# Optimization experiments

Hardware: AMD Instinct MI355X
Metric: run time of the kernel (lower is better)

## Reference

```python
import jax, jax.numpy as jnp
import numpy as np

UNITS = 50

def setup_inputs() -> dict:
    key = jax.random.key(0)
    ks = jax.random.split(key, 6)
    B, T, F = 4096, 128, 64
    scale = 0.1
    return {
        "x": jax.random.normal(ks[0], (B, T, F), dtype=jnp.float32),
        "W": jax.random.normal(ks[1], (F, 3 * UNITS), dtype=jnp.float32) * scale,
        "U": jax.random.normal(ks[2], (UNITS, 3 * UNITS), dtype=jnp.float32) * scale,
        "b": jax.random.normal(ks[3], (2, 3 * UNITS), dtype=jnp.float32) * scale,
        "Wd": jax.random.normal(ks[4], (UNITS, 1), dtype=jnp.float32) * scale,
        "bd": jnp.zeros((1,), dtype=jnp.float32),
    }

def reference(x, W, U, b, Wd, bd):
    # Keras GRU, reset_after=True, activation=relu, recurrent_activation=sigmoid.
    B, T, F = x.shape
    u = UNITS
    # Precompute input projections for all timesteps: [B,T,3u]
    xp = jnp.einsum('btf,fk->btk', x, W) + b[0]
    xp = jnp.moveaxis(xp, 1, 0)  # [T,B,3u]
    bi = b[1]

    def step(h, xt):
        hp = h @ U + bi                     # [B,3u]
        xz, xr, xh = xt[:, :u], xt[:, u:2*u], xt[:, 2*u:]
        hz, hr, hh = hp[:, :u], hp[:, u:2*u], hp[:, 2*u:]
        z = jax.nn.sigmoid(xz + hz)
        r = jax.nn.sigmoid(xr + hr)
        hcand = jax.nn.relu(xh + r * hh)
        h_new = z * h + (1.0 - z) * hcand
        return h_new, None

    h0 = jnp.zeros((B, u), dtype=x.dtype)
    hT, _ = jax.lax.scan(step, h0, xp)
    # Dropout is identity at inference; Dense head:
    return hT @ Wd + bd
```

## Files before the change

kernel.cpp:

```cpp
#include <hip/hip_runtime.h>
#include <math.h>

typedef _Float16 v8h __attribute__((ext_vector_type(8)));
typedef float v4f __attribute__((ext_vector_type(4)));

#define UNITS    50
#define K3       150
#define FDIM     64
#define TSTEPS   128
#define BATCH    4096
#define NB       16
#define H16S     72
#define H32S     52

#if __has_builtin(__builtin_amdgcn_exp2f)
__device__ __forceinline__ float fast_exp2(float x) { return __builtin_amdgcn_exp2f(x); }
#else
__device__ __forceinline__ float fast_exp2(float x) { return exp2f(x); }
#endif
#if __has_builtin(__builtin_amdgcn_rcpf)
__device__ __forceinline__ float fast_rcp(float x) { return __builtin_amdgcn_rcpf(x); }
#else
__device__ __forceinline__ float fast_rcp(float x) { return 1.0f / x; }
#endif

__global__ __launch_bounds__(256, 1)
void gru_4w(const float* __restrict__ x, const float* __restrict__ W,
            const float* __restrict__ U, const float* __restrict__ bv,
            const float* __restrict__ Wd, const float* __restrict__ bd,
            float* __restrict__ out) {
    __shared__ _Float16 hs16[2][NB * H16S];
    __shared__ float    hs32[NB * H32S];

    const int tid  = threadIdx.x;
    const int nt   = tid >> 6;
    const int lane = tid & 63;
    const int n    = lane & 15;
    const int quad = lane >> 4;
    const int b0   = blockIdx.x * NB;
    const int c    = nt * 16 + n;

    for (int i = tid; i < NB * H16S; i += 256) {
        _Float16 v = ((i % H16S) == 50) ? (_Float16)1.f : (_Float16)0.f;
        hs16[0][i] = v;
        hs16[1][i] = v;
    }

    v8h Bz[4], Br[4], Bh[4];
    #pragma unroll
    for (int kt = 0; kt < 4; ++kt) {
        v8h fz, fr, fh;
        #pragma unroll
        for (int j = 0; j < 8; ++j) {
            const int k = kt * 32 + quad * 8 + j;
            float vz = 0.f, vr = 0.f, vh = 0.f;
            if (c < UNITS) {
                if (k < FDIM) {
                    vz = W[k * K3 + c];
                    vr = W[k * K3 + 50 + c];
                    vh = W[k * K3 + 100 + c];
                } else if (k < FDIM + UNITS) {
                    const int ur = k - FDIM;
                    vz = U[ur * K3 + c];
                    vr = U[ur * K3 + 50 + c];
                    vh = U[ur * K3 + 100 + c];
                } else if (k == FDIM + UNITS) {
                    vh = bv[250 + c];
                }
            }
            fz[j] = (_Float16)vz; fr[j] = (_Float16)vr; fh[j] = (_Float16)vh;
        }
        Bz[kt] = fz; Br[kt] = fr; Bh[kt] = fh;
    }

    const float CE = -1.44269504f;
    float bzc = 0.f, brc = 0.f, bx = 0.f;
    if (c < UNITS) {
        bzc = CE * (bv[c]      + bv[150 + c]);
        brc = CE * (bv[50 + c] + bv[200 + c]);
        bx  = bv[100 + c];
    }

    v4f h32 = {0.f, 0.f, 0.f, 0.f};

    const float* xbase = x + ((size_t)(b0 + n) * TSTEPS) * FDIM + quad * 8;
    v4f px0 = *(const v4f*)(xbase + 0);
    v4f px1 = *(const v4f*)(xbase + 4);
    v4f px2 = *(const v4f*)(xbase + 32);
    v4f px3 = *(const v4f*)(xbase + 36);

    __syncthreads();

    for (int t = 0; t < TSTEPS; ++t) {
        const _Float16* hrd = hs16[t & 1];
        _Float16*       hwr = hs16[(t + 1) & 1];

        v8h A0, A1;
        #pragma unroll
        for (int j = 0; j < 4; ++j) {
            A0[j]     = (_Float16)px0[j];
            A0[j + 4] = (_Float16)px1[j];
            A1[j]     = (_Float16)px2[j];
            A1[j + 4] = (_Float16)px3[j];
        }
        v8h A2 = *(const v8h*)(&hrd[n * H16S + quad * 8]);
        v8h A3 = *(const v8h*)(&hrd[n * H16S + 32 + quad * 8]);

        if (t + 1 < TSTEPS) {
            const float* xp = xbase + (size_t)(t + 1) * FDIM;
            px0 = *(const v4f*)(xp + 0);
            px1 = *(const v4f*)(xp + 4);
            px2 = *(const v4f*)(xp + 32);
            px3 = *(const v4f*)(xp + 36);
        }

        const v4f zero4 = {0.f, 0.f, 0.f, 0.f};
        v4f ax = {bx, bx, bx, bx};
        v4f az = __builtin_amdgcn_mfma_f32_16x16x32_f16(A0, Bz[0], zero4, 0, 0, 0);
        az     = __builtin_amdgcn_mfma_f32_16x16x32_f16(A1, Bz[1], az,    0, 0, 0);
        v4f ar = __builtin_amdgcn_mfma_f32_16x16x32_f16(A0, Br[0], zero4, 0, 0, 0);
        ar     = __builtin_amdgcn_mfma_f32_16x16x32_f16(A1, Br[1], ar,    0, 0, 0);
        ax     = __builtin_amdgcn_mfma_f32_16x16x32_f16(A0, Bh[0], ax,    0, 0, 0);
        ax     = __builtin_amdgcn_mfma_f32_16x16x32_f16(A1, Bh[1], ax,    0, 0, 0);
        az     = __builtin_amdgcn_mfma_f32_16x16x32_f16(A2, Bz[2], az,    0, 0, 0);
        az     = __builtin_amdgcn_mfma_f32_16x16x32_f16(A3, Bz[3], az,    0, 0, 0);
        ar     = __builtin_amdgcn_mfma_f32_16x16x32_f16(A2, Br[2], ar,    0, 0, 0);
        ar     = __builtin_amdgcn_mfma_f32_16x16x32_f16(A3, Br[3], ar,    0, 0, 0);
        v4f ah = __builtin_amdgcn_mfma_f32_16x16x32_f16(A2, Bh[2], zero4, 0, 0, 0);
        ah     = __builtin_amdgcn_mfma_f32_16x16x32_f16(A3, Bh[3], ah,    0, 0, 0);

        #pragma unroll
        for (int r = 0; r < 4; ++r) {
            const float ez = fast_exp2(fmaf(az[r], CE, bzc));
            const float er = fast_exp2(fmaf(ar[r], CE, brc));
            const float pz = 1.f + ez;
            const float pr = 1.f + er;
            const float d  = fast_rcp(pz * pr);
            const float zg = d * pr;
            const float rg = d * pz;
            const float hc = fmaxf(fmaf(rg, ah[r], ax[r]), 0.f);
            const float hn = fmaf(zg, h32[r] - hc, hc);
            h32[r] = hn;
            if (c < UNITS)
                hwr[(quad * 4 + r) * H16S + c] = (_Float16)hn;
        }
        __syncthreads();
    }

    if (c < UNITS) {
        #pragma unroll
        for (int r = 0; r < 4; ++r)
            hs32[(quad * 4 + r) * H32S + c] = h32[r];
    }
    __syncthreads();
    if (tid < NB) {
        float acc = bd[0];
        #pragma unroll
        for (int u = 0; u < UNITS; ++u)
            acc = fmaf(hs32[tid * H32S + u], Wd[u], acc);
        out[b0 + tid] = acc;
    }
}

extern "C" void kernel_launch(void* const* d_in, const int* in_sizes, int n_in,
                              void* d_out, int out_size, void* d_ws, size_t ws_size,
                              hipStream_t stream) {
    const float* x    = (const float*)d_in[0];
    const float* W    = (const float*)d_in[1];
    const float* U    = (const float*)d_in[2];
    const float* bv   = (const float*)d_in[3];
    const float* Wd   = (const float*)d_in[4];
    const float* bd   = (const float*)d_in[5];
    float* out = (float*)d_out;

    dim3 grid(BATCH / NB);
    dim3 block(256);
    gru_4w<<<grid, block, 0, stream>>>(x, W, U, bv, Wd, bd, out);
}
```

Baseline: 272.6 us.

## Software-pipeline input projection MFMAs one step ahead and deepen x prefetch

Moves the x-dependent MFMAs for step t+1 into step t, after the recurrent MFMAs are issued, so they overlap the gate math and stay off the h-dependent critical path. The x prefetch now reaches two steps ahead using alternating register buffers and a loop unrolled by two. __syncthreads is replaced by an explicit lgkmcnt wait plus s_barrier and sched_barrier. This costs extra registers for the prefetched x and the partial accumulators, and the hand-written barrier is a correctness risk if any memory ordering was relied on.

```diff
diff --git a/kernel.cpp b/kernel.cpp
--- a/kernel.cpp
+++ b/kernel.cpp
@@ -84,50 +84,72 @@
     v4f h32 = {0.f, 0.f, 0.f, 0.f};
 
     const float* xbase = x + ((size_t)(b0 + n) * TSTEPS) * FDIM + quad * 8;
-    v4f px0 = *(const v4f*)(xbase + 0);
-    v4f px1 = *(const v4f*)(xbase + 4);
-    v4f px2 = *(const v4f*)(xbase + 32);
-    v4f px3 = *(const v4f*)(xbase + 36);
+
+    v4f az_x, ar_x, ax_x;
+    auto xpart = [&](const v4f& q0, const v4f& q1, const v4f& q2, const v4f& q3) {
+        v8h A0, A1;
+        #pragma unroll
+        for (int j = 0; j < 4; ++j) {
+            A0[j]     = (_Float16)q0[j];
+            A0[j + 4] = (_Float16)q1[j];
+            A1[j]     = (_Float16)q2[j];
+            A1[j + 4] = (_Float16)q3[j];
+        }
+        const v4f zero4 = {0.f, 0.f, 0.f, 0.f};
+        az_x = __builtin_amdgcn_mfma_f32_16x16x32_f16(A0, Bz[0], zero4, 0, 0, 0);
+        az_x = __builtin_amdgcn_mfma_f32_16x16x32_f16(A1, Bz[1], az_x,  0, 0, 0);
+        ar_x = __builtin_amdgcn_mfma_f32_16x16x32_f16(A0, Br[0], zero4, 0, 0, 0);
+        ar_x = __builtin_amdgcn_mfma_f32_16x16x32_f16(A1, Br[1], ar_x,  0, 0, 0);
+        v4f axi = {bx, bx, bx, bx};
+        ax_x = __builtin_amdgcn_mfma_f32_16x16x32_f16(A0, Bh[0], axi,  0, 0, 0);
+        ax_x = __builtin_amdgcn_mfma_f32_16x16x32_f16(A1, Bh[1], ax_x, 0, 0, 0);
+    };
+
+    {
+        v4f q0 = *(const v4f*)(xbase + 0);
+        v4f q1 = *(const v4f*)(xbase + 4);
+        v4f q2 = *(const v4f*)(xbase + 32);
+        v4f q3 = *(const v4f*)(xbase + 36);
+        xpart(q0, q1, q2, q3);
+    }
+    v4f pxO[4], pxE[4];
+    {
+        const float* x1 = xbase + (size_t)1 * FDIM;
+        pxO[0] = *(const v4f*)(x1 + 0);  pxO[1] = *(const v4f*)(x1 + 4);
+        pxO[2] = *(const v4f*)(x1 + 32); pxO[3] = *(const v4f*)(x1 + 36);
+        const float* x2 = xbase + (size_t)2 * FDIM;
+        pxE[0] = *(const v4f*)(x2 + 0);  pxE[1] = *(const v4f*)(x2 + 4);
+        pxE[2] = *(const v4f*)(x2 + 32); pxE[3] = *(const v4f*)(x2 + 36);
+    }
 
     __syncthreads();
 
-    for (int t = 0; t < TSTEPS; ++t) {
+    auto step = [&](int t, v4f (&px)[4]) {
         const _Float16* hrd = hs16[t & 1];
         _Float16*       hwr = hs16[(t + 1) & 1];
 
-        v8h A0, A1;
-        #pragma unroll
-        for (int j = 0; j < 4; ++j) {
-            A0[j]     = (_Float16)px0[j];
-            A0[j + 4] = (_Float16)px1[j];
-            A1[j]     = (_Float16)px2[j];
-            A1[j + 4] = (_Float16)px3[j];
-        }
         v8h A2 = *(const v8h*)(&hrd[n * H16S + quad * 8]);
         v8h A3 = *(const v8h*)(&hrd[n * H16S + 32 + quad * 8]);
 
-        if (t + 1 < TSTEPS) {
-            const float* xp = xbase + (size_t)(t + 1) * FDIM;
-            px0 = *(const v4f*)(xp + 0);
-            px1 = *(const v4f*)(xp + 4);
-            px2 = *(const v4f*)(xp + 32);
-            px3 = *(const v4f*)(xp + 36);
-        }
-
         const v4f zero4 = {0.f, 0.f, 0.f, 0.f};
-        v4f ax = {bx, bx, bx, bx};
-        v4f az = __builtin_amdgcn_mfma_f32_16x16x32_f16(A0, Bz[0], zero4, 0, 0, 0);
-        az     = __builtin_amdgcn_mfma_f32_16x16x32_f16(A1, Bz[1], az,    0, 0, 0);
-        v4f ar = __builtin_amdgcn_mfma_f32_16x16x32_f16(A0, Br[0], zero4, 0, 0, 0);
-        ar     = __builtin_amdgcn_mfma_f32_16x16x32_f16(A1, Br[1], ar,    0, 0, 0);
-        ax     = __builtin_amdgcn_mfma_f32_16x16x32_f16(A0, Bh[0], ax,    0, 0, 0);
-        ax     = __builtin_amdgcn_mfma_f32_16x16x32_f16(A1, Bh[1], ax,    0, 0, 0);
-        az     = __builtin_amdgcn_mfma_f32_16x16x32_f16(A2, Bz[2], az,    0, 0, 0);
-        az     = __builtin_amdgcn_mfma_f32_16x16x32_f16(A3, Bz[3], az,    0, 0, 0);
-        ar     = __builtin_amdgcn_mfma_f32_16x16x32_f16(A2, Br[2], ar,    0, 0, 0);
-        ar     = __builtin_amdgcn_mfma_f32_16x16x32_f16(A3, Br[3], ar,    0, 0, 0);
+        v4f az = __builtin_amdgcn_mfma_f32_16x16x32_f16(A2, Bz[2], az_x, 0, 0, 0);
+        az     = __builtin_amdgcn_mfma_f32_16x16x32_f16(A3, Bz[3], az,   0, 0, 0);
+        v4f ar = __builtin_amdgcn_mfma_f32_16x16x32_f16(A2, Br[2], ar_x, 0, 0, 0);
+        ar     = __builtin_amdgcn_mfma_f32_16x16x32_f16(A3, Br[3], ar,   0, 0, 0);
         v4f ah = __builtin_amdgcn_mfma_f32_16x16x32_f16(A2, Bh[2], zero4, 0, 0, 0);
         ah     = __builtin_amdgcn_mfma_f32_16x16x32_f16(A3, Bh[3], ah,    0, 0, 0);
+        v4f ax = ax_x;
+
+        if (t + 1 < TSTEPS) {
+            xpart(px[0], px[1], px[2], px[3]);
+            if (t + 3 < TSTEPS) {
+                const float* xp = xbase + (size_t)(t + 3) * FDIM;
+                px[0] = *(const v4f*)(xp + 0);
+                px[1] = *(const v4f*)(xp + 4);
+                px[2] = *(const v4f*)(xp + 32);
+                px[3] = *(const v4f*)(xp + 36);
+            }
+        }
 
         #pragma unroll
         for (int r = 0; r < 4; ++r) {
@@ -144,7 +166,15 @@
             if (c < UNITS)
                 hwr[(quad * 4 + r) * H16S + c] = (_Float16)hn;
         }
-        __syncthreads();
+
+        asm volatile("s_waitcnt lgkmcnt(0)" ::: "memory");
+        __builtin_amdgcn_s_barrier();
+        __builtin_amdgcn_sched_barrier(0);
+    };
+
+    for (int t = 0; t < TSTEPS; t += 2) {
+        step(t,     pxO);
+        step(t + 1, pxE);
     }
 
     if (c < UNITS) {
```

New measurement: 274.2 us. No clear change (+0.6%).

## Run each batch tile in one wave with transposed MFMA and register-resident state

Applied to the files above, without the earlier changes.

Replaces the 4-wave block, which exchanged the hidden state through shared memory and a barrier every step, with a single 64-lane wave per 16-row batch tile. The GEMM is transposed so the weights act as the A operand and the batch as B, letting each lane's hidden-state outputs feed straight into the next step's B operand without LDS or __syncthreads. The z/r biases are folded into the matmul through a constant-one input, x loads are prefetched two steps ahead with a step pair unrolled, and the dense head is reduced with cross-lane shuffles. The cost is four times as many MFMAs per wave, large register pressure from holding 48 weight fragments, and only one wave per block.

```diff
diff --git a/kernel.cpp b/kernel.cpp
--- a/kernel.cpp
+++ b/kernel.cpp
@@ -10,8 +10,6 @@
 #define TSTEPS   128
 #define BATCH    4096
 #define NB       16
-#define H16S     72
-#define H32S     52
 
 #if __has_builtin(__builtin_amdgcn_exp2f)
 __device__ __forceinline__ float fast_exp2(float x) { return __builtin_amdgcn_exp2f(x); }
@@ -24,142 +22,164 @@
 __device__ __forceinline__ float fast_rcp(float x) { return 1.0f / x; }
 #endif
 
-__global__ __launch_bounds__(256, 1)
-void gru_4w(const float* __restrict__ x, const float* __restrict__ W,
+__global__ __launch_bounds__(64, 1)
+void gru_1w(const float* __restrict__ x, const float* __restrict__ W,
             const float* __restrict__ U, const float* __restrict__ bv,
             const float* __restrict__ Wd, const float* __restrict__ bd,
             float* __restrict__ out) {
-    __shared__ _Float16 hs16[2][NB * H16S];
-    __shared__ float    hs32[NB * H32S];
+    const int lane = threadIdx.x & 63;
+    const int n    = lane & 15;
+    const int q    = lane >> 4;
+    const int b0   = blockIdx.x * NB;
 
-    const int tid  = threadIdx.x;
-    const int nt   = tid >> 6;
-    const int lane = tid & 63;
-    const int n    = lane & 15;
-    const int quad = lane >> 4;
-    const int b0   = blockIdx.x * NB;
-    const int c    = nt * 16 + n;
-
-    for (int i = tid; i < NB * H16S; i += 256) {
-        _Float16 v = ((i % H16S) == 50) ? (_Float16)1.f : (_Float16)0.f;
-        hs16[0][i] = v;
-        hs16[1][i] = v;
+    v8h Az[4][4], Ar[4][4], Ah[4][4];
+    #pragma unroll
+    for (int mt = 0; mt < 4; ++mt) {
+        const int m = mt * 16 + n;
+        const bool mreal = (m < UNITS);
+        #pragma unroll
+        for (int kt = 0; kt < 4; ++kt) {
+            v8h fz, fr, fh;
+            #pragma unroll
+            for (int j = 0; j < 8; ++j) {
+                float vz = 0.f, vr = 0.f, vh = 0.f;
+                if (mreal) {
+                    if (kt < 2) {
+                        const int feat = kt * 32 + q * 8 + j;
+                        vz = W[feat * K3 + m];
+                        vr = W[feat * K3 + 50 + m];
+                        vh = W[feat * K3 + 100 + m];
+                    } else if (kt == 3 && q == 0 && j == 6) {
+                        vz = bv[m]      + bv[150 + m];
+                        vr = bv[50 + m] + bv[200 + m];
+                        vh = bv[250 + m];
+                    } else {
+                        const int u = ((kt - 2) * 2 + (j >> 2)) * 16 + q * 4 + (j & 3);
+                        if (u < UNITS) {
+                            vz = U[u * K3 + m];
+                            vr = U[u * K3 + 50 + m];
+                            vh = U[u * K3 + 100 + m];
+                        }
+                    }
+                }
+                fz[j] = (_Float16)vz; fr[j] = (_Float16)vr; fh[j] = (_Float16)vh;
+            }
+            Az[mt][kt] = fz; Ar[mt][kt] = fr; Ah[mt][kt] = fh;
+        }
     }
 
-    v8h Bz[4], Br[4], Bh[4];
+    v4f bx4[4];
     #pragma unroll
-    for (int kt = 0; kt < 4; ++kt) {
-        v8h fz, fr, fh;
+    for (int mt = 0; mt < 4; ++mt)
         #pragma unroll
-        for (int j = 0; j < 8; ++j) {
-            const int k = kt * 32 + quad * 8 + j;
-            float vz = 0.f, vr = 0.f, vh = 0.f;
-            if (c < UNITS) {
-                if (k < FDIM) {
-                    vz = W[k * K3 + c];
-                    vr = W[k * K3 + 50 + c];
-                    vh = W[k * K3 + 100 + c];
-                } else if (k < FDIM + UNITS) {
-                    const int ur = k - FDIM;
-                    vz = U[ur * K3 + c];
-                    vr = U[ur * K3 + 50 + c];
-                    vh = U[ur * K3 + 100 + c];
-                } else if (k == FDIM + UNITS) {
-                    vh = bv[250 + c];
-                }
-            }
-            fz[j] = (_Float16)vz; fr[j] = (_Float16)vr; fh[j] = (_Float16)vh;
+        for (int r = 0; r < 4; ++r) {
+            const int u = mt * 16 + q * 4 + r;
+            bx4[mt][r] = (u < UNITS) ? bv[100 + u] : 0.f;
         }
-        Bz[kt] = fz; Br[kt] = fr; Bh[kt] = fh;
+
+    const float CE = -1.44269504f;
+
+    v4f h32[4];
+    #pragma unroll
+    for (int mt = 0; mt < 4; ++mt) h32[mt] = v4f{0.f, 0.f, 0.f, 0.f};
+
+    const float* xb = x + ((size_t)(b0 + n) * TSTEPS) * FDIM + q * 8;
+    v4f pxA[4], pxB[4];
+    pxA[0] = *(const v4f*)(xb + 0);  pxA[1] = *(const v4f*)(xb + 4);
+    pxA[2] = *(const v4f*)(xb + 32); pxA[3] = *(const v4f*)(xb + 36);
+    {
+        const float* x1 = xb + (size_t)FDIM;
+        pxB[0] = *(const v4f*)(x1 + 0);  pxB[1] = *(const v4f*)(x1 + 4);
+        pxB[2] = *(const v4f*)(x1 + 32); pxB[3] = *(const v4f*)(x1 + 36);
     }
 
-    const float CE = -1.44269504f;
-    float bzc = 0.f, brc = 0.f, bx = 0.f;
-    if (c < UNITS) {
-        bzc = CE * (bv[c]      + bv[150 + c]);
-        brc = CE * (bv[50 + c] + bv[200 + c]);
-        bx  = bv[100 + c];
+    auto step = [&](int t, v4f (&px)[4]) {
+        v8h B0, B1;
+        #pragma unroll
+        for (int j = 0; j < 4; ++j) {
+            B0[j]     = (_Float16)px[0][j];
+            B0[j + 4] = (_Float16)px[1][j];
+            B1[j]     = (_Float16)px[2][j];
+            B1[j + 4] = (_Float16)px[3][j];
+        }
+        const v4f z4 = {0.f, 0.f, 0.f, 0.f};
+        v4f Cz[4], Cr[4], Chx[4], Chh[4];
+        #pragma unroll
+        for (int mt = 0; mt < 4; ++mt) {
+            Cz[mt]  = __builtin_amdgcn_mfma_f32_16x16x32_f16(Az[mt][0], B0, z4,       0, 0, 0);
+            Cr[mt]  = __builtin_amdgcn_mfma_f32_16x16x32_f16(Ar[mt][0], B0, z4,       0, 0, 0);
+            Chx[mt] = __builtin_amdgcn_mfma_f32_16x16x32_f16(Ah[mt][0], B0, bx4[mt],  0, 0, 0);
+        }
+        #pragma unroll
+        for (int mt = 0; mt < 4; ++mt) {
+            Cz[mt]  = __builtin_amdgcn_mfma_f32_16x16x32_f16(Az[mt][1], B1, Cz[mt],  0, 0, 0);
+            Cr[mt]  = __builtin_amdgcn_mfma_f32_16x16x32_f16(Ar[mt][1], B1, Cr[mt],  0, 0, 0);
+            Chx[mt] = __builtin_amdgcn_mfma_f32_16x16x32_f16(Ah[mt][1], B1, Chx[mt], 0, 0, 0);
+        }
+        if (t + 2 < TSTEPS) {
+            const float* xp = xb + (size_t)(t + 2) * FDIM;
+            px[0] = *(const v4f*)(xp + 0);
+            px[1] = *(const v4f*)(xp + 4);
+            px[2] = *(const v4f*)(xp + 32);
+            px[3] = *(const v4f*)(xp + 36);
+        }
+        v8h B2, B3;
+        #pragma unroll
+        for (int j = 0; j < 8; ++j) B2[j] = (_Float16)h32[j >> 2][j & 3];
+        B3[0] = (_Float16)h32[2][0]; B3[1] = (_Float16)h32[2][1];
+        B3[2] = (_Float16)h32[2][2]; B3[3] = (_Float16)h32[2][3];
+        B3[4] = (_Float16)h32[3][0]; B3[5] = (_Float16)h32[3][1];
+        B3[6] = (q == 0) ? (_Float16)1.f : (_Float16)0.f;
+        B3[7] = (_Float16)0.f;
+        #pragma unroll
+        for (int mt = 0; mt < 4; ++mt) {
+            Cz[mt]  = __builtin_amdgcn_mfma_f32_16x16x32_f16(Az[mt][2], B2, Cz[mt],  0, 0, 0);
+            Cr[mt]  = __builtin_amdgcn_mfma_f32_16x16x32_f16(Ar[mt][2], B2, Cr[mt],  0, 0, 0);
+            Chh[mt] = __builtin_amdgcn_mfma_f32_16x16x32_f16(Ah[mt][2], B2, z4,      0, 0, 0);
+        }
+        #pragma unroll
+        for (int mt = 0; mt < 4; ++mt) {
+            Cz[mt]  = __builtin_amdgcn_mfma_f32_16x16x32_f16(Az[mt][3], B3, Cz[mt],  0, 0, 0);
+            Cr[mt]  = __builtin_amdgcn_mfma_f32_16x16x32_f16(Ar[mt][3], B3, Cr[mt],  0, 0, 0);
+            Chh[mt] = __builtin_amdgcn_mfma_f32_16x16x32_f16(Ah[mt][3], B3, Chh[mt], 0, 0, 0);
+        }
+        #pragma unroll
+        for (int mt = 0; mt < 4; ++mt) {
+            #pragma unroll
+            for (int r = 0; r < 4; ++r) {
+                if (mt == 3 && r >= 2) continue;
+                const float ez = fast_exp2(Cz[mt][r] * CE);
+                const float er = fast_exp2(Cr[mt][r] * CE);
+                const float pz = 1.f + ez;
+                const float pr = 1.f + er;
+                const float d  = fast_rcp(pz * pr);
+                const float zg = d * pr;
+                const float rg = d * pz;
+                const float hc = fmaxf(fmaf(rg, Chh[mt][r], Chx[mt][r]), 0.f);
+                h32[mt][r] = fmaf(zg, h32[mt][r] - hc, hc);
+            }
+        }
+    };
+
+    #pragma unroll 1
+    for (int t = 0; t < TSTEPS; t += 2) {
+        step(t,     pxA);
+        step(t + 1, pxB);
     }
 
-    v4f h32 = {0.f, 0.f, 0.f, 0.f};
-
-    const float* xbase = x + ((size_t)(b0 + n) * TSTEPS) * FDIM + quad * 8;
-    v4f px0 = *(const v4f*)(xbase + 0);
-    v4f px1 = *(const v4f*)(xbase + 4);
-    v4f px2 = *(const v4f*)(xbase + 32);
-    v4f px3 = *(const v4f*)(xbase + 36);
-
-    __syncthreads();
-
-    for (int t = 0; t < TSTEPS; ++t) {
-        const _Float16* hrd = hs16[t & 1];
-        _Float16*       hwr = hs16[(t + 1) & 1];
-
-        v8h A0, A1;
-        #pragma unroll
-        for (int j = 0; j < 4; ++j) {
-            A0[j]     = (_Float16)px0[j];
-            A0[j + 4] = (_Float16)px1[j];
-            A1[j]     = (_Float16)px2[j];
-            A1[j + 4] = (_Float16)px3[j];
-        }
-        v8h A2 = *(const v8h*)(&hrd[n * H16S + quad * 8]);
-        v8h A3 = *(const v8h*)(&hrd[n * H16S + 32 + quad * 8]);
-
-        if (t + 1 < TSTEPS) {
-            const float* xp = xbase + (size_t)(t + 1) * FDIM;
-            px0 = *(const v4f*)(xp + 0);
-            px1 = *(const v4f*)(xp + 4);
-            px2 = *(const v4f*)(xp + 32);
-            px3 = *(const v4f*)(xp + 36);
-        }
-
-        const v4f zero4 = {0.f, 0.f, 0.f, 0.f};
-        v4f ax = {bx, bx, bx, bx};
-        v4f az = __builtin_amdgcn_mfma_f32_16x16x32_f16(A0, Bz[0], zero4, 0, 0, 0);
-        az     = __builtin_amdgcn_mfma_f32_16x16x32_f16(A1, Bz[1], az,    0, 0, 0);
-        v4f ar = __builtin_amdgcn_mfma_f32_16x16x32_f16(A0, Br[0], zero4, 0, 0, 0);
-        ar     = __builtin_amdgcn_mfma_f32_16x16x32_f16(A1, Br[1], ar,    0, 0, 0);
-        ax     = __builtin_amdgcn_mfma_f32_16x16x32_f16(A0, Bh[0], ax,    0, 0, 0);
-        ax     = __builtin_amdgcn_mfma_f32_16x16x32_f16(A1, Bh[1], ax,    0, 0, 0);
-        az     = __builtin_amdgcn_mfma_f32_16x16x32_f16(A2, Bz[2], az,    0, 0, 0);
-        az     = __builtin_amdgcn_mfma_f32_16x16x32_f16(A3, Bz[3], az,    0, 0, 0);
-        ar     = __builtin_amdgcn_mfma_f32_16x16x32_f16(A2, Br[2], ar,    0, 0, 0);
-        ar     = __builtin_amdgcn_mfma_f32_16x16x32_f16(A3, Br[3], ar,    0, 0, 0);
-        v4f ah = __builtin_amdgcn_mfma_f32_16x16x32_f16(A2, Bh[2], zero4, 0, 0, 0);
-        ah     = __builtin_amdgcn_mfma_f32_16x16x32_f16(A3, Bh[3], ah,    0, 0, 0);
-
-        #pragma unroll
-        for (int r = 0; r < 4; ++r) {
-            const float ez = fast_exp2(fmaf(az[r], CE, bzc));
-            const float er = fast_exp2(fmaf(ar[r], CE, brc));
-            const float pz = 1.f + ez;
-            const float pr = 1.f + er;
-            const float d  = fast_rcp(pz * pr);
-            const float zg = d * pr;
-            const float rg = d * pz;
-            const float hc = fmaxf(fmaf(rg, ah[r], ax[r]), 0.f);
-            const float hn = fmaf(zg, h32[r] - hc, hc);
-            h32[r] = hn;
-            if (c < UNITS)
-                hwr[(quad * 4 + r) * H16S + c] = (_Float16)hn;
-        }
-        __syncthreads();
-    }
-
-    if (c < UNITS) {
+    float acc = 0.f;
+    #pragma unroll
+    for (int mt = 0; mt < 3; ++mt)
         #pragma unroll
         for (int r = 0; r < 4; ++r)
-            hs32[(quad * 4 + r) * H32S + c] = h32[r];
+            acc = fmaf(h32[mt][r], Wd[mt * 16 + q * 4 + r], acc);
+    if (q == 0) {
+        acc = fmaf(h32[3][0], Wd[48], acc);
+        acc = fmaf(h32[3][1], Wd[49], acc);
     }
-    __syncthreads();
-    if (tid < NB) {
-        float acc = bd[0];
-        #pragma unroll
-        for (int u = 0; u < UNITS; ++u)
-            acc = fmaf(hs32[tid * H32S + u], Wd[u], acc);
-        out[b0 + tid] = acc;
-    }
+    acc += __shfl_xor(acc, 16, 64);
+    acc += __shfl_xor(acc, 32, 64);
+    if (q == 0) out[b0 + n] = acc + bd[0];
 }
 
 extern "C" void kernel_launch(void* const* d_in, const int* in_sizes, int n_in,
@@ -174,6 +194,6 @@
     float* out = (float*)d_out;
 
     dim3 grid(BATCH / NB);
-    dim3 block(256);
-    gru_4w<<<grid, block, 0, stream>>>(x, W, U, bv, Wd, bd, out);
+    dim3 block(64);
+    gru_1w<<<grid, block, 0, stream>>>(x, W, U, bv, Wd, bd, out);
 }
```

Result: slower. 312.9 us (+14.8%).
